# Performance work log

Measured on AMD Instinct MI355X. Metric: run time of the kernel, lower is better.

Reference implementation:

```python
import jax, jax.numpy as jnp
import numpy as np

N_NODES = 100000
N_EDGES = 1600000
D = 8                      # node_channels_in = [D, D]
PROD = D * D               # 64
MSG_DIM = 128
IN_MSG = 2 * PROD + 2 * 2 + 2 * 1   # 134
MSG_OUT = 2 * D            # 16
IN_EIG = 2 * D + 2 * D     # node_channels_sum + 2*D = 32


def setup_inputs() -> dict:
    key = jax.random.key(0)
    ks = jax.random.split(key, 12)
    a = jax.random.normal(ks[0], (N_NODES, D, D), dtype=jnp.float32)
    h_i = 0.5 * (a + jnp.swapaxes(a, -1, -2))  # symmetric so eigh is valid
    edge_index = jax.random.randint(ks[1], (2, N_EDGES), 0, N_NODES)
    node_params = jax.random.normal(ks[2], (N_NODES, 2), dtype=jnp.float32)
    edge_params = jax.random.normal(ks[3], (N_EDGES, 1), dtype=jnp.float32)
    s = 0.05
    return {
        "h_i": h_i,
        "node_params": node_params,
        "edge_params": edge_params,
        "W1": jax.random.normal(ks[4], (IN_MSG, MSG_DIM), dtype=jnp.float32) * s,
        "b1": jnp.zeros((MSG_DIM,), dtype=jnp.float32),
        "W2": jax.random.normal(ks[5], (MSG_DIM, MSG_OUT), dtype=jnp.float32) * s,
        "b2": jnp.zeros((MSG_OUT,), dtype=jnp.float32),
        "W3": jax.random.normal(ks[6], (IN_EIG, MSG_DIM), dtype=jnp.float32) * s,
        "b3": jnp.zeros((MSG_DIM,), dtype=jnp.float32),
        "W4": jax.random.normal(ks[7], (MSG_DIM, D), dtype=jnp.float32) * s,
        "b4": jnp.zeros((D,), dtype=jnp.float32),
        "edge_index": edge_index,
    }


def reference(h_i, node_params, edge_params, W1, b1, W2, b2, W3, b3, W4, b4, edge_index):
    sender = edge_index[0]
    receiver = edge_index[1]
    E = sender.shape[0]
    N = node_params.shape[0]

    # gather + flatten node states per edge: [E, D*D]
    h_s = h_i[sender].reshape(E, -1)
    h_r = h_i[receiver].reshape(E, -1)
    # faithful to torch: edge_params[edge_index] -> [2, E, 1] then view(E, -1) -> [E, 2]
    ep = edge_params[edge_index].reshape(E, -1)

    cat = jnp.concatenate(
        [h_s, h_r, node_params[sender], node_params[receiver], ep], axis=1
    )  # [E, 134]

    # phi_message_Real: Linear -> SiLU -> Linear -> SiLU
    hidden = jax.nn.silu(cat @ W1 + b1)          # [E, 128]
    I_ij = jax.nn.silu(hidden @ W2 + b2)         # [E, 16]

    # scatter_add over receiver
    agg = jax.ops.segment_sum(I_ij, receiver, num_segments=N)  # [N, 16]

    # eigh-based update
    eigvals, eigvecs = jnp.linalg.eigh(h_i)          # [N, D], [N, D, D]
    mags = jnp.linalg.norm(eigvecs, axis=-1)         # [N, D] (row norms, as torch.norm(dim=-1))

    feats = jnp.concatenate([agg, eigvals, mags], axis=1)  # [N, 32]
    lam = jax.nn.softmax(jax.nn.silu(feats @ W3 + b3) @ W4 + b4, axis=-1)  # [N, D]

    # V diag(lam) V^T  per node
    h_updated = jnp.einsum("nij,nj,nkj->nik", eigvecs, lam, eigvecs)
    return h_updated
```

## Files before the change

### kernel.cpp

```cpp
#include <hip/hip_runtime.h>
#include <math.h>

typedef __attribute__((ext_vector_type(8))) short bf16x8;
typedef __attribute__((ext_vector_type(4))) float f32x4;
typedef _Float16 half2v __attribute__((ext_vector_type(2)));

__device__ __forceinline__ float silu(float x) {
    return x / (1.0f + __expf(-x));
}

__device__ __forceinline__ unsigned short f2bf(float x) {
    union { float f; unsigned u; } v; v.f = x;
    unsigned r = v.u + 0x7fffu + ((v.u >> 16) & 1u);
    return (unsigned short)(r >> 16);
}

__device__ __forceinline__ unsigned pack2(float a, float b) {
    return (unsigned)f2bf(a) | ((unsigned)f2bf(b) << 16);
}

__device__ __forceinline__ unsigned pack2h(float a, float b) {
    half2v h; h[0] = (_Float16)a; h[1] = (_Float16)b;
    return __builtin_bit_cast(unsigned, h);
}

__device__ __forceinline__ unsigned cvt_pk(float lo, float hi) {
    unsigned r;
    asm("v_cvt_pk_bf16_f32 %0, %1, %2" : "=v"(r) : "v"(lo), "v"(hi));
    return r;
}

__global__ __launch_bounds__(256)
void k_prep(const float* __restrict__ np,
            const float* __restrict__ ep,
            const int* __restrict__ eidx,
            unsigned* __restrict__ npp,
            unsigned* __restrict__ epk,
            int N, int E)
{
    const int tid = blockIdx.x * 256 + threadIdx.x;
    const int gs = gridDim.x * 256;
    for (int i = tid; i < N; i += gs)
        npp[i] = pack2(np[2 * i], np[2 * i + 1]);
    for (int i = tid; i < E; i += gs)
        epk[i] = pack2h(ep[eidx[2 * i]], ep[eidx[2 * i + 1]]);
}

__global__ __launch_bounds__(256)
void k_pre(const float* __restrict__ h_i,
           const unsigned* __restrict__ npp,
           const float* __restrict__ W1, const float* __restrict__ b1,
           unsigned short* __restrict__ SAB, int N)
{
    const int t = threadIdx.x;
    const int lane = t & 63;
    const int wv = t >> 6;
    const int lr = lane & 15;
    const int lq = lane >> 4;

    bf16x8 aw[4][3];
    #pragma unroll
    for (int mf = 0; mf < 4; ++mf) {
        const int c = wv * 64 + mf * 16 + lr;
        const bool isA = c < 128;
        const int col = c & 127;
        #pragma unroll
        for (int ks = 0; ks < 3; ++ks) {
            bf16x8 w;
            #pragma unroll
            for (int j = 0; j < 8; ++j) {
                const int kl = lq * 8 + j;
                float v = 0.0f;
                if (ks < 2) {
                    const int kk = ks * 32 + kl;
                    v = W1[(size_t)(isA ? kk : 64 + kk) * 128 + col];
                } else if (kl < 2) {
                    v = W1[(size_t)((isA ? 128 : 130) + kl) * 128 + col];
                }
                w[j] = (short)f2bf(v);
            }
            aw[mf][ks] = w;
        }
    }
    float4 b1v[4];
    #pragma unroll
    for (int mf = 0; mf < 4; ++mf) {
        if (wv < 2) b1v[mf] = *(const float4*)&b1[wv * 64 + mf * 16 + lq * 4];
        else        b1v[mf] = make_float4(0.f, 0.f, 0.f, 0.f);
    }

    const int nTiles = (N + 15) / 16;
    for (int tile = blockIdx.x; tile < nTiles; tile += gridDim.x) {
        const int n  = tile * 16 + lr;
        const int nc = (n < N) ? n : (N - 1);

        const float* hr = h_i + (size_t)nc * 64;
        bf16x8 B0, B1, B2;
        {
            float4 a0 = *(const float4*)&hr[lq * 8];
            float4 a1 = *(const float4*)&hr[lq * 8 + 4];
            float4 a2 = *(const float4*)&hr[32 + lq * 8];
            float4 a3 = *(const float4*)&hr[32 + lq * 8 + 4];
            unsigned u[4];
            u[0] = pack2(a0.x, a0.y); u[1] = pack2(a0.z, a0.w);
            u[2] = pack2(a1.x, a1.y); u[3] = pack2(a1.z, a1.w);
            B0 = __builtin_bit_cast(bf16x8, *(uint4*)u);
            u[0] = pack2(a2.x, a2.y); u[1] = pack2(a2.z, a2.w);
            u[2] = pack2(a3.x, a3.y); u[3] = pack2(a3.z, a3.w);
            B1 = __builtin_bit_cast(bf16x8, *(uint4*)u);
            unsigned z[4] = {0u, 0u, 0u, 0u};
            if (lq == 0) z[0] = npp[nc];
            B2 = __builtin_bit_cast(bf16x8, *(uint4*)z);
        }

        f32x4 acc[4];
        #pragma unroll
        for (int mf = 0; mf < 4; ++mf) {
            acc[mf] = (f32x4){0.f, 0.f, 0.f, 0.f};
            acc[mf] = __builtin_amdgcn_mfma_f32_16x16x32_bf16(aw[mf][0], B0, acc[mf], 0, 0, 0);
            acc[mf] = __builtin_amdgcn_mfma_f32_16x16x32_bf16(aw[mf][1], B1, acc[mf], 0, 0, 0);
            acc[mf] = __builtin_amdgcn_mfma_f32_16x16x32_bf16(aw[mf][2], B2, acc[mf], 0, 0, 0);
        }

        if (n < N) {
            unsigned short* row = SAB + (size_t)n * 256;
            #pragma unroll
            for (int mf = 0; mf < 4; ++mf) {
                uint2 u;
                u.x = pack2h(acc[mf][0] + b1v[mf].x, acc[mf][1] + b1v[mf].y);
                u.y = pack2h(acc[mf][2] + b1v[mf].z, acc[mf][3] + b1v[mf].w);
                *(uint2*)&row[wv * 64 + mf * 16 + lq * 4] = u;
            }
        }
    }
}

__global__ __launch_bounds__(256, 3)
void k_edge_v5(const unsigned short* __restrict__ SAB,
               const unsigned* __restrict__ epk,
               const int* __restrict__ eidx,
               const float* __restrict__ W1,
               const float* __restrict__ W2, const float* __restrict__ b2,
               float* __restrict__ agg,
               int N, int E)
{
    const int t = threadIdx.x;
    const int lane = t & 63;
    const int wv = t >> 6;
    const int lr = lane & 15;
    const int lq = lane >> 4;

    half2v wA[4][4], wB[4][4];
    #pragma unroll
    for (int ks = 0; ks < 4; ++ks)
        #pragma unroll
        for (int c = 0; c < 4; ++c) {
            const int d = ks * 32 + lq * 8 + 2 * c;
            half2v a; a[0] = (_Float16)W1[132 * 128 + d]; a[1] = (_Float16)W1[132 * 128 + d + 1];
            half2v b; b[0] = (_Float16)W1[133 * 128 + d]; b[1] = (_Float16)W1[133 * 128 + d + 1];
            wA[ks][c] = a; wB[ks][c] = b;
        }

    bf16x8 bw2[4];
    #pragma unroll
    for (int ks = 0; ks < 4; ++ks) {
        bf16x8 w;
        #pragma unroll
        for (int j = 0; j < 8; ++j) {
            const int k = ks * 32 + lq * 8 + j;
            w[j] = (short)f2bf(W2[(size_t)k * 16 + lr]);
        }
        bw2[ks] = w;
    }
    const float bias2 = b2[lr];

    const uint4* S4 = (const uint4*)SAB;
    const int nG = (E + 15) / 16;
    const int gstride = gridDim.x * 4;
    int g = blockIdx.x * 4 + wv;
    if (g >= nG) return;

    int s0, r0; unsigned ep0; int rc0[4];
    uint4 A0[4], B0[4];
    {
        const int eb = g * 16;
        const int e = eb + lr; const int ec = (e < E) ? e : (E - 1);
        s0 = eidx[ec]; r0 = eidx[E + ec]; ep0 = epk[ec];
        if (eb + 16 <= E) {
            const int4 rv = *(const int4*)&eidx[E + eb + lq * 4];
            rc0[0] = rv.x; rc0[1] = rv.y; rc0[2] = rv.z; rc0[3] = rv.w;
        } else {
            #pragma unroll
            for (int r2 = 0; r2 < 4; ++r2) {
                int e4 = eb + lq * 4 + r2;
                rc0[r2] = eidx[E + ((e4 < E) ? e4 : (E - 1))];
            }
        }
        const uint4* pa = S4 + (size_t)s0 * 32;
        const uint4* pb = S4 + (size_t)r0 * 32 + 16;
        #pragma unroll
        for (int ks = 0; ks < 4; ++ks) { A0[ks] = pa[ks * 4 + lq]; B0[ks] = pb[ks * 4 + lq]; }
    }

    for (; g < nG; g += gstride) {
        const int gn = g + gstride;
        const bool hn = gn < nG;

        int s1 = 0, r1 = 0; unsigned ep1 = 0; int rc1[4] = {0, 0, 0, 0};
        if (hn) {
            const int eb = gn * 16;
            const int e = eb + lr; const int ec = (e < E) ? e : (E - 1);
            s1 = eidx[ec]; r1 = eidx[E + ec]; ep1 = epk[ec];
            if (eb + 16 <= E) {
                const int4 rv = *(const int4*)&eidx[E + eb + lq * 4];
                rc1[0] = rv.x; rc1[1] = rv.y; rc1[2] = rv.z; rc1[3] = rv.w;
            } else {
                #pragma unroll
                for (int r2 = 0; r2 < 4; ++r2) {
                    int e4 = eb + lq * 4 + r2;
                    rc1[r2] = eidx[E + ((e4 < E) ? e4 : (E - 1))];
                }
            }
        }

        const unsigned elo = (ep0 & 0xffffu) | (ep0 << 16);
        const unsigned ehi = (ep0 >> 16) | (ep0 & 0xffff0000u);
        const half2v e0 = __builtin_bit_cast(half2v, elo);
        const half2v e1 = __builtin_bit_cast(half2v, ehi);

        bf16x8 af[4];
        #pragma unroll
        for (int ks = 0; ks < 4; ++ks) {
            unsigned w[4];
            const unsigned* ua = (const unsigned*)&A0[ks];
            const unsigned* ub = (const unsigned*)&B0[ks];
            #pragma unroll
            for (int c = 0; c < 4; ++c) {
                half2v v = __builtin_bit_cast(half2v, ua[c])
                         + __builtin_bit_cast(half2v, ub[c]);
                v = wA[ks][c] * e0 + v;
                v = wB[ks][c] * e1 + v;
                const float x0 = (float)v[0];
                const float x1 = (float)v[1];
                w[c] = cvt_pk(silu(x0), silu(x1));
            }
            af[ks] = __builtin_bit_cast(bf16x8, *(uint4*)w);
        }

        uint4 A1[4], B1[4];
        if (hn) {
            const uint4* pa = S4 + (size_t)s1 * 32;
            const uint4* pb = S4 + (size_t)r1 * 32 + 16;
            #pragma unroll
            for (int ks = 0; ks < 4; ++ks) { A1[ks] = pa[ks * 4 + lq]; B1[ks] = pb[ks * 4 + lq]; }
        }

        f32x4 acc = (f32x4){0.f, 0.f, 0.f, 0.f};
        #pragma unroll
        for (int ks = 0; ks < 4; ++ks)
            acc = __builtin_amdgcn_mfma_f32_16x16x32_bf16(af[ks], bw2[ks], acc, 0, 0, 0);

        const int eb = g * 16;
        if (eb + 16 <= E) {
            #pragma unroll
            for (int r2 = 0; r2 < 4; ++r2)
                atomicAdd(&agg[(size_t)rc0[r2] * 16 + lr], silu(acc[r2] + bias2));
        } else {
            #pragma unroll
            for (int r2 = 0; r2 < 4; ++r2)
                if (eb + lq * 4 + r2 < E)
                    atomicAdd(&agg[(size_t)rc0[r2] * 16 + lr], silu(acc[r2] + bias2));
        }

        if (hn) {
            s0 = s1; r0 = r1; ep0 = ep1;
            #pragma unroll
            for (int r2 = 0; r2 < 4; ++r2) rc0[r2] = rc1[r2];
            #pragma unroll
            for (int ks = 0; ks < 4; ++ks) { A0[ks] = A1[ks]; B0[ks] = B1[ks]; }
        }
    }
}

__host__ __device__ constexpr int tix(int i, int j) {
    return (i <= j) ? (i * 8 - (i * (i + 1)) / 2 + j)
                    : (j * 8 - (j * (j + 1)) / 2 + i);
}

template <int P, int Q>
__device__ __forceinline__ void jrot(float* T, float* V) {
    const float app = T[tix(P, P)];
    const float aqq = T[tix(Q, Q)];
    const float apq = T[tix(P, Q)];

    float theta = (aqq - app) / (2.0f * apq);
    float at = fabsf(theta);
    float tt = 1.0f / (at + sqrtf(at * at + 1.0f));
    tt = (theta < 0.0f) ? -tt : tt;
    float cc = __frsqrt_rn(tt * tt + 1.0f);
    float ss = tt * cc;

    const bool skip = !(fabsf(apq) > 1e-36f);
    const float c  = skip ? 1.0f : cc;
    const float s  = skip ? 0.0f : ss;
    const float tu = skip ? 0.0f : tt;

    #pragma unroll
    for (int k = 0; k < 8; ++k) {
        if (k == P || k == Q) continue;
        const float akp = T[tix(k, P)], akq = T[tix(k, Q)];
        T[tix(k, P)] = c * akp - s * akq;
        T[tix(k, Q)] = s * akp + c * akq;
    }
    T[tix(P, P)] = app - tu * apq;
    T[tix(Q, Q)] = aqq + tu * apq;
    T[tix(P, Q)] = 0.0f;

    #pragma unroll
    for (int k = 0; k < 8; ++k) {
        const float vp = V[k * 8 + P], vq = V[k * 8 + Q];
        V[k * 8 + P] = c * vp - s * vq;
        V[k * 8 + Q] = s * vp + c * vq;
    }
}

__device__ __forceinline__ void jacobi_sweep(float* T, float* V) {
    jrot<0,1>(T,V); jrot<0,2>(T,V); jrot<0,3>(T,V); jrot<0,4>(T,V);
    jrot<0,5>(T,V); jrot<0,6>(T,V); jrot<0,7>(T,V);
    jrot<1,2>(T,V); jrot<1,3>(T,V); jrot<1,4>(T,V); jrot<1,5>(T,V);
    jrot<1,6>(T,V); jrot<1,7>(T,V);
    jrot<2,3>(T,V); jrot<2,4>(T,V); jrot<2,5>(T,V); jrot<2,6>(T,V);
    jrot<2,7>(T,V);
    jrot<3,4>(T,V); jrot<3,5>(T,V); jrot<3,6>(T,V); jrot<3,7>(T,V);
    jrot<4,5>(T,V); jrot<4,6>(T,V); jrot<4,7>(T,V);
    jrot<5,6>(T,V); jrot<5,7>(T,V);
    jrot<6,7>(T,V);
}

#define CSWAP(a, b)                                                          \
    {                                                                        \
        bool sw = eig[a] > eig[b];                                           \
        float lo = sw ? eig[b] : eig[a];                                     \
        float hi = sw ? eig[a] : eig[b];                                     \
        eig[a] = lo; eig[b] = hi;                                            \
        _Pragma("unroll")                                                    \
        for (int k = 0; k < 8; ++k) {                                        \
            float va = V[k * 8 + a], vb = V[k * 8 + b];                      \
            V[k * 8 + a] = sw ? vb : va;                                     \
            V[k * 8 + b] = sw ? va : vb;                                     \
        }                                                                    \
    }

__global__ __launch_bounds__(64)
void k_node(const float* __restrict__ h_i,
            const float* __restrict__ agg,
            const float* __restrict__ W3, const float* __restrict__ b3,
            const float* __restrict__ W4, const float* __restrict__ b4,
            float* __restrict__ out, int N)
{
    const int n = blockIdx.x * 64 + threadIdx.x;
    if (n >= N) return;

    float T[36], V[64];
    {
        float A[64];
        const float4* src = (const float4*)(h_i + (size_t)n * 64);
        #pragma unroll
        for (int i = 0; i < 16; ++i) ((float4*)A)[i] = src[i];
        #pragma unroll
        for (int i = 0; i < 8; ++i)
            #pragma unroll
            for (int j = 0; j < 8; ++j)
                if (i <= j) T[tix(i, j)] = A[i * 8 + j];
    }
    #pragma unroll
    for (int i = 0; i < 64; ++i) V[i] = 0.0f;
    #pragma unroll
    for (int i = 0; i < 8; ++i) V[i * 8 + i] = 1.0f;

    #pragma unroll 1
    for (int sw = 0; sw < 5; ++sw) jacobi_sweep(T, V);

    float eig[8];
    #pragma unroll
    for (int i = 0; i < 8; ++i) eig[i] = T[tix(i, i)];

    CSWAP(0,1) CSWAP(2,3) CSWAP(4,5) CSWAP(6,7)
    CSWAP(0,2) CSWAP(1,3) CSWAP(4,6) CSWAP(5,7)
    CSWAP(1,2) CSWAP(5,6)
    CSWAP(0,4) CSWAP(1,5) CSWAP(2,6) CSWAP(3,7)
    CSWAP(2,4) CSWAP(3,5)
    CSWAP(1,2) CSWAP(3,4) CSWAP(5,6)

    float f[32];
    {
        const float4* ag = (const float4*)(agg + (size_t)n * 16);
        #pragma unroll
        for (int i = 0; i < 4; ++i) {
            float4 v = ag[i];
            f[i * 4 + 0] = v.x; f[i * 4 + 1] = v.y;
            f[i * 4 + 2] = v.z; f[i * 4 + 3] = v.w;
        }
    }
    #pragma unroll
    for (int i = 0; i < 8; ++i) f[16 + i] = eig[i];
    #pragma unroll
    for (int i = 0; i < 8; ++i) f[24 + i] = 1.0f;

    float z[8];
    #pragma unroll
    for (int o = 0; o < 8; ++o) z[o] = b4[o];
    #pragma unroll 1
    for (int j = 0; j < 128; ++j) {
        float h = b3[j];
        #pragma unroll
        for (int k = 0; k < 32; ++k) h += f[k] * W3[k * 128 + j];
        const float sv = silu(h);
        #pragma unroll
        for (int o = 0; o < 8; ++o) z[o] += sv * W4[j * 8 + o];
    }

    float m = z[0];
    #pragma unroll
    for (int o = 1; o < 8; ++o) m = fmaxf(m, z[o]);
    float lam[8], den = 0.0f;
    #pragma unroll
    for (int o = 0; o < 8; ++o) { lam[o] = __expf(z[o] - m); den += lam[o]; }
    const float inv = 1.0f / den;
    #pragma unroll
    for (int o = 0; o < 8; ++o) lam[o] *= inv;

    float* orow = out + (size_t)n * 64;
    #pragma unroll
    for (int i = 0; i < 8; ++i) {
        float si[8];
        #pragma unroll
        for (int j = 0; j < 8; ++j) si[j] = lam[j] * V[i * 8 + j];
        float r[8];
        #pragma unroll
        for (int k = 0; k < 8; ++k) {
            float sum = 0.0f;
            #pragma unroll
            for (int j = 0; j < 8; ++j) sum += si[j] * V[k * 8 + j];
            r[k] = sum;
        }
        ((float4*)orow)[i * 2 + 0] = make_float4(r[0], r[1], r[2], r[3]);
        ((float4*)orow)[i * 2 + 1] = make_float4(r[4], r[5], r[6], r[7]);
    }
}

#define CATS 168
#define HS   136
__global__ __launch_bounds__(256, 2)
void k_edge_v2(const float* __restrict__ h_i,
               const float* __restrict__ node_params,
               const float* __restrict__ edge_params,
               const float* __restrict__ W1, const float* __restrict__ b1,
               const float* __restrict__ W2, const float* __restrict__ b2,
               const int* __restrict__ eidx,
               float* __restrict__ agg,
               int N, int E)
{
    __shared__ unsigned short smem[23680];
    unsigned short* w1t = smem;
    unsigned short* w2t = smem + 128 * CATS;
    unsigned short* cat = smem;
    unsigned short* hid = smem + 64 * CATS;

    const int t = threadIdx.x;
    const int lane = t & 63;
    const int wv = t >> 6;
    const int wn = wv & 1;
    const int wm = wv >> 1;
    const int lr = lane & 15;
    const int lq = lane >> 4;

    for (int idx = t; idx < 128 * 80; idx += 256) {
        const int col = idx & 127, kp = idx >> 7;
        const int k0 = 2 * kp;
        float f0 = (k0     < 134) ? W1[(size_t)k0       * 128 + col] : 0.0f;
        float f1 = (k0 + 1 < 134) ? W1[(size_t)(k0 + 1) * 128 + col] : 0.0f;
        *(unsigned*)&w1t[col * CATS + k0] = pack2(f0, f1);
    }
    for (int idx = t; idx < 16 * 64; idx += 256) {
        const int col = idx & 15, kp = idx >> 4;
        const int k0 = 2 * kp;
        *(unsigned*)&w2t[col * HS + k0] =
            pack2(W2[(size_t)k0 * 16 + col], W2[(size_t)(k0 + 1) * 16 + col]);
    }
    __syncthreads();

    bf16x8 bw1[4][5];
    #pragma unroll
    for (int nf = 0; nf < 4; ++nf)
        #pragma unroll
        for (int ks = 0; ks < 5; ++ks)
            bw1[nf][ks] = *(const bf16x8*)&w1t[(wn * 64 + nf * 16 + lr) * CATS + ks * 32 + lq * 8];
    bf16x8 bw2[4];
    #pragma unroll
    for (int ks = 0; ks < 4; ++ks)
        bw2[ks] = *(const bf16x8*)&w2t[lr * HS + ks * 32 + lq * 8];

    float bias1[4];
    #pragma unroll
    for (int nf = 0; nf < 4; ++nf) bias1[nf] = b1[wn * 64 + nf * 16 + lr];
    const float bias2 = b2[lr];
    __syncthreads();

    const int el = t >> 2;
    const int p  = t & 3;

    const int nTiles = E / 64;
    for (int tile = blockIdx.x; tile < nTiles; tile += gridDim.x) {
        const int ebase = tile * 64;
        {
            const int eg  = ebase + el;
            const int egc = (eg < E) ? eg : (E - 1);
            const int s = eidx[egc];
            const int r = eidx[E + egc];
            const float4* hs = (const float4*)(h_i + (size_t)s * 64);
            const float4* hr = (const float4*)(h_i + (size_t)r * 64);
            unsigned short* crow = cat + el * CATS;
            #pragma unroll
            for (int m = 0; m < 8; ++m) {
                const int q = p + 4 * m;
                float4 v = (q < 16) ? hs[q] : hr[q - 16];
                uint2 u; u.x = pack2(v.x, v.y); u.y = pack2(v.z, v.w);
                *(uint2*)&crow[q * 4] = u;
            }
            if (p == 0) {
                const int i0 = eidx[2 * egc];
                const int i1 = eidx[2 * egc + 1];
                uint4 u;
                u.x = pack2(node_params[2 * s], node_params[2 * s + 1]);
                u.y = pack2(node_params[2 * r], node_params[2 * r + 1]);
                u.z = pack2(edge_params[i0], edge_params[i1]);
                u.w = 0u;
                *(uint4*)&crow[128] = u;
            } else {
                uint4 z; z.x = z.y = z.z = z.w = 0u;
                *(uint4*)&crow[136 + (p - 1) * 8] = z;
            }
        }
        __syncthreads();

        f32x4 acc[2][4];
        #pragma unroll
        for (int mf = 0; mf < 2; ++mf)
            #pragma unroll
            for (int nf = 0; nf < 4; ++nf)
                acc[mf][nf] = (f32x4){0.f, 0.f, 0.f, 0.f};

        const unsigned short* pa = cat + (wm * 32 + lr) * CATS + lq * 8;
        #pragma unroll
        for (int ks = 0; ks < 5; ++ks) {
            const bf16x8 a0 = *(const bf16x8*)(pa + ks * 32);
            const bf16x8 a1 = *(const bf16x8*)(pa + 16 * CATS + ks * 32);
            #pragma unroll
            for (int nf = 0; nf < 4; ++nf) {
                acc[0][nf] = __builtin_amdgcn_mfma_f32_16x16x32_bf16(a0, bw1[nf][ks], acc[0][nf], 0, 0, 0);
                acc[1][nf] = __builtin_amdgcn_mfma_f32_16x16x32_bf16(a1, bw1[nf][ks], acc[1][nf], 0, 0, 0);
            }
        }
        __syncthreads();

        #pragma unroll
        for (int mf = 0; mf < 2; ++mf)
            #pragma unroll
            for (int nf = 0; nf < 4; ++nf) {
                const float bb = bias1[nf];
                #pragma unroll
                for (int r2 = 0; r2 < 4; ++r2) {
                    const float x = acc[mf][nf][r2] + bb;
                    hid[(wm * 32 + mf * 16 + lq * 4 + r2) * HS + wn * 64 + nf * 16 + lr] =
                        f2bf(silu(x));
                }
            }
        __syncthreads();

        f32x4 acc2 = (f32x4){0.f, 0.f, 0.f, 0.f};
        const unsigned short* ph = hid + (wv * 16 + lr) * HS + lq * 8;
        #pragma unroll
        for (int ks = 0; ks < 4; ++ks)
            acc2 = __builtin_amdgcn_mfma_f32_16x16x32_bf16(
                *(const bf16x8*)(ph + ks * 32), bw2[ks], acc2, 0, 0, 0);

        #pragma unroll
        for (int r2 = 0; r2 < 4; ++r2) {
            const int eg2 = ebase + wv * 16 + lq * 4 + r2;
            if (eg2 < E) {
                const int rcv = eidx[E + eg2];
                const float v = silu(acc2[r2] + bias2);
                atomicAdd(&agg[(size_t)rcv * 16 + lr], v);
            }
        }
        __syncthreads();
    }
}

extern "C" void kernel_launch(void* const* d_in, const int* in_sizes, int n_in,
                              void* d_out, int out_size, void* d_ws, size_t ws_size,
                              hipStream_t stream) {
    const float* h_i  = (const float*)d_in[0];
    const float* npar = (const float*)d_in[1];
    const float* epar = (const float*)d_in[2];
    const float* W1   = (const float*)d_in[3];
    const float* b1   = (const float*)d_in[4];
    const float* W2   = (const float*)d_in[5];
    const float* b2   = (const float*)d_in[6];
    const float* W3   = (const float*)d_in[7];
    const float* b3   = (const float*)d_in[8];
    const float* W4   = (const float*)d_in[9];
    const float* b4   = (const float*)d_in[10];
    const int*   eidx = (const int*)d_in[11];

    const int N = in_sizes[0] / 64;
    const int E = in_sizes[11] / 2;

    const size_t aggB = (size_t)N * 16 * sizeof(float);
    size_t off = (aggB + 255) & ~(size_t)255;
    const size_t sabOff = off;                  off += (size_t)N * 256 * 2;
    off = (off + 255) & ~(size_t)255;
    const size_t epkOff = off;                  off += (size_t)E * 4;
    off = (off + 255) & ~(size_t)255;
    const size_t nppOff = off;                  off += (size_t)N * 4;
    const size_t need = off;

    float* agg = (float*)d_ws;
    hipMemsetAsync(agg, 0, aggB, stream);

    if (ws_size >= need) {
        unsigned short* SAB = (unsigned short*)((char*)d_ws + sabOff);
        unsigned* epk = (unsigned*)((char*)d_ws + epkOff);
        unsigned* npp = (unsigned*)((char*)d_ws + nppOff);

        k_prep<<<1024, 256, 0, stream>>>(npar, epar, eidx, npp, epk, N, E);
        k_pre<<<1024, 256, 0, stream>>>(h_i, npp, W1, b1, SAB, N);
        k_edge_v5<<<768, 256, 0, stream>>>(SAB, epk, eidx, W1, W2, b2,
                                           agg, N, E);
    } else {
        int blocks = E / 64;
        if (blocks > 768) blocks = 768;
        k_edge_v2<<<blocks, 256, 0, stream>>>(h_i, npar, epar, W1, b1, W2, b2,
                                              eidx, agg, N, E);
    }
    k_node<<<(N + 63) / 64, 64, 0, stream>>>(h_i, agg, W3, b3, W4, b4,
                                             (float*)d_out, N);
}
```

Measured before the change: 323.7 us.

## Use MFMA for node MLP, merge prep kernels, enlarge edge grid

The per-node scalar MLP (32→128→8) in the node kernel is replaced with fp16 MFMA tiles staged through shared memory, with 256-thread blocks. k_prep and k_pre are merged into one launch whose extra blocks pack the edge params, and node params are packed inline, which drops the npp buffer. The edge kernel grid grows from 768 to 2048 blocks. fp16 weights and activations in the node MLP cost precision, and the larger node blocks may hurt occupancy given the heavy Jacobi register use.

```diff
diff --git a/kernel.cpp b/kernel.cpp
--- a/kernel.cpp
+++ b/kernel.cpp
@@ -4,6 +4,7 @@
 typedef __attribute__((ext_vector_type(8))) short bf16x8;
 typedef __attribute__((ext_vector_type(4))) float f32x4;
 typedef _Float16 half2v __attribute__((ext_vector_type(2)));
+typedef _Float16 f16x8 __attribute__((ext_vector_type(8)));
 
 __device__ __forceinline__ float silu(float x) {
     return x / (1.0f + __expf(-x));
@@ -31,27 +32,23 @@
 }
 
 __global__ __launch_bounds__(256)
-void k_prep(const float* __restrict__ np,
+void k_pre2(const float* __restrict__ h_i,
+            const float* __restrict__ np,
             const float* __restrict__ ep,
             const int* __restrict__ eidx,
-            unsigned* __restrict__ npp,
+            const float* __restrict__ W1, const float* __restrict__ b1,
+            unsigned short* __restrict__ SAB,
             unsigned* __restrict__ epk,
             int N, int E)
 {
-    const int tid = blockIdx.x * 256 + threadIdx.x;
-    const int gs = gridDim.x * 256;
-    for (int i = tid; i < N; i += gs)
-        npp[i] = pack2(np[2 * i], np[2 * i + 1]);
-    for (int i = tid; i < E; i += gs)
-        epk[i] = pack2h(ep[eidx[2 * i]], ep[eidx[2 * i + 1]]);
-}
-
-__global__ __launch_bounds__(256)
-void k_pre(const float* __restrict__ h_i,
-           const unsigned* __restrict__ npp,
-           const float* __restrict__ W1, const float* __restrict__ b1,
-           unsigned short* __restrict__ SAB, int N)
-{
+    if (blockIdx.x >= 1024) {
+        const int tid = (blockIdx.x - 1024) * 256 + threadIdx.x;
+        const int gs = 512 * 256;
+        for (int i = tid; i < E; i += gs)
+            epk[i] = pack2h(ep[eidx[2 * i]], ep[eidx[2 * i + 1]]);
+        return;
+    }
+
     const int t = threadIdx.x;
     const int lane = t & 63;
     const int wv = t >> 6;
@@ -90,7 +87,7 @@
     }
 
     const int nTiles = (N + 15) / 16;
-    for (int tile = blockIdx.x; tile < nTiles; tile += gridDim.x) {
+    for (int tile = blockIdx.x; tile < nTiles; tile += 1024) {
         const int n  = tile * 16 + lr;
         const int nc = (n < N) ? n : (N - 1);
 
@@ -109,7 +106,7 @@
             u[2] = pack2(a3.x, a3.y); u[3] = pack2(a3.z, a3.w);
             B1 = __builtin_bit_cast(bf16x8, *(uint4*)u);
             unsigned z[4] = {0u, 0u, 0u, 0u};
-            if (lq == 0) z[0] = npp[nc];
+            if (lq == 0) z[0] = pack2(np[2 * nc], np[2 * nc + 1]);
             B2 = __builtin_bit_cast(bf16x8, *(uint4*)z);
         }
 
@@ -351,20 +348,30 @@
         }                                                                    \
     }
 
-__global__ __launch_bounds__(64)
-void k_node(const float* __restrict__ h_i,
-            const float* __restrict__ agg,
-            const float* __restrict__ W3, const float* __restrict__ b3,
-            const float* __restrict__ W4, const float* __restrict__ b4,
-            float* __restrict__ out, int N)
+__global__ __launch_bounds__(256)
+void k_node2(const float* __restrict__ h_i,
+             const float* __restrict__ agg,
+             const float* __restrict__ W3, const float* __restrict__ b3,
+             const float* __restrict__ W4, const float* __restrict__ b4,
+             float* __restrict__ out, int N)
 {
-    const int n = blockIdx.x * 64 + threadIdx.x;
-    if (n >= N) return;
+    __shared__ _Float16 fl[4][64][40];
+    __shared__ _Float16 hl[4][16][136];
+    __shared__ float    zl[4][64][8];
+
+    const int t = threadIdx.x;
+    const int lane = t & 63;
+    const int wv = t >> 6;
+    const int lr = lane & 15;
+    const int lq = lane >> 4;
+
+    const int n  = blockIdx.x * 256 + t;
+    const int nc = (n < N) ? n : (N - 1);
 
     float T[36], V[64];
     {
         float A[64];
-        const float4* src = (const float4*)(h_i + (size_t)n * 64);
+        const float4* src = (const float4*)(h_i + (size_t)nc * 64);
         #pragma unroll
         for (int i = 0; i < 16; ++i) ((float4*)A)[i] = src[i];
         #pragma unroll
@@ -392,34 +399,89 @@
     CSWAP(2,4) CSWAP(3,5)
     CSWAP(1,2) CSWAP(3,4) CSWAP(5,6)
 
-    float f[32];
+    f16x8 w3f[8];
+    #pragma unroll
+    for (int nf = 0; nf < 8; ++nf) {
+        f16x8 w;
+        #pragma unroll
+        for (int j = 0; j < 8; ++j)
+            w[j] = (_Float16)W3[(size_t)(lq * 8 + j) * 128 + nf * 16 + lr];
+        w3f[nf] = w;
+    }
+    f16x8 w4f[4];
+    #pragma unroll
+    for (int ks = 0; ks < 4; ++ks) {
+        f16x8 w;
+        #pragma unroll
+        for (int j = 0; j < 8; ++j)
+            w[j] = (lr < 8) ? (_Float16)W4[(size_t)(ks * 32 + lq * 8 + j) * 8 + lr]
+                            : (_Float16)0.0f;
+        w4f[ks] = w;
+    }
+    float b3v[8];
+    #pragma unroll
+    for (int nf = 0; nf < 8; ++nf) b3v[nf] = b3[nf * 16 + lr];
+    const float b4v = (lr < 8) ? b4[lr] : 0.0f;
+
     {
-        const float4* ag = (const float4*)(agg + (size_t)n * 16);
+        float f[32];
+        const float4* ag = (const float4*)(agg + (size_t)nc * 16);
         #pragma unroll
         for (int i = 0; i < 4; ++i) {
             float4 v = ag[i];
             f[i * 4 + 0] = v.x; f[i * 4 + 1] = v.y;
             f[i * 4 + 2] = v.z; f[i * 4 + 3] = v.w;
         }
-    }
-    #pragma unroll
-    for (int i = 0; i < 8; ++i) f[16 + i] = eig[i];
-    #pragma unroll
-    for (int i = 0; i < 8; ++i) f[24 + i] = 1.0f;
+        #pragma unroll
+        for (int i = 0; i < 8; ++i) f[16 + i] = eig[i];
+        #pragma unroll
+        for (int i = 0; i < 8; ++i) f[24 + i] = 1.0f;
+
+        unsigned* dst = (unsigned*)&fl[wv][lane][0];
+        #pragma unroll
+        for (int i = 0; i < 16; ++i) dst[i] = pack2h(f[2 * i], f[2 * i + 1]);
+    }
+    __syncthreads();
+
+    #pragma unroll 1
+    for (int b = 0; b < 4; ++b) {
+        const f16x8 a1 = *(const f16x8*)&fl[wv][b * 16 + lr][lq * 8];
+        f32x4 acc1[8];
+        #pragma unroll
+        for (int nf = 0; nf < 8; ++nf) {
+            acc1[nf] = (f32x4){0.f, 0.f, 0.f, 0.f};
+            acc1[nf] = __builtin_amdgcn_mfma_f32_16x16x32_f16(a1, w3f[nf], acc1[nf], 0, 0, 0);
+        }
+        #pragma unroll
+        for (int nf = 0; nf < 8; ++nf)
+            #pragma unroll
+            for (int r2 = 0; r2 < 4; ++r2) {
+                const float x = acc1[nf][r2] + b3v[nf];
+                hl[wv][lq * 4 + r2][nf * 16 + lr] = (_Float16)silu(x);
+            }
+        __syncthreads();
+
+        f32x4 acc2 = (f32x4){0.f, 0.f, 0.f, 0.f};
+        #pragma unroll
+        for (int ks = 0; ks < 4; ++ks) {
+            const f16x8 a2 = *(const f16x8*)&hl[wv][lr][ks * 32 + lq * 8];
+            acc2 = __builtin_amdgcn_mfma_f32_16x16x32_f16(a2, w4f[ks], acc2, 0, 0, 0);
+        }
+        if (lr < 8) {
+            #pragma unroll
+            for (int r2 = 0; r2 < 4; ++r2)
+                zl[wv][b * 16 + lq * 4 + r2][lr] = acc2[r2] + b4v;
+        }
+        __syncthreads();
+    }
 
     float z[8];
-    #pragma unroll
-    for (int o = 0; o < 8; ++o) z[o] = b4[o];
-    #pragma unroll 1
-    for (int j = 0; j < 128; ++j) {
-        float h = b3[j];
-        #pragma unroll
-        for (int k = 0; k < 32; ++k) h += f[k] * W3[k * 128 + j];
-        const float sv = silu(h);
-        #pragma unroll
-        for (int o = 0; o < 8; ++o) z[o] += sv * W4[j * 8 + o];
-    }
-
+    {
+        float4 z0 = *(const float4*)&zl[wv][lane][0];
+        float4 z1 = *(const float4*)&zl[wv][lane][4];
+        z[0] = z0.x; z[1] = z0.y; z[2] = z0.z; z[3] = z0.w;
+        z[4] = z1.x; z[5] = z1.y; z[6] = z1.z; z[7] = z1.w;
+    }
     float m = z[0];
     #pragma unroll
     for (int o = 1; o < 8; ++o) m = fmaxf(m, z[o]);
@@ -430,22 +492,24 @@
     #pragma unroll
     for (int o = 0; o < 8; ++o) lam[o] *= inv;
 
-    float* orow = out + (size_t)n * 64;
-    #pragma unroll
-    for (int i = 0; i < 8; ++i) {
-        float si[8];
-        #pragma unroll
-        for (int j = 0; j < 8; ++j) si[j] = lam[j] * V[i * 8 + j];
-        float r[8];
-        #pragma unroll
-        for (int k = 0; k < 8; ++k) {
-            float sum = 0.0f;
-            #pragma unroll
-            for (int j = 0; j < 8; ++j) sum += si[j] * V[k * 8 + j];
-            r[k] = sum;
-        }
-        ((float4*)orow)[i * 2 + 0] = make_float4(r[0], r[1], r[2], r[3]);
-        ((float4*)orow)[i * 2 + 1] = make_float4(r[4], r[5], r[6], r[7]);
+    if (n < N) {
+        float* orow = out + (size_t)n * 64;
+        #pragma unroll
+        for (int i = 0; i < 8; ++i) {
+            float si[8];
+            #pragma unroll
+            for (int j = 0; j < 8; ++j) si[j] = lam[j] * V[i * 8 + j];
+            float r[8];
+            #pragma unroll
+            for (int k = 0; k < 8; ++k) {
+                float sum = 0.0f;
+                #pragma unroll
+                for (int j = 0; j < 8; ++j) sum += si[j] * V[k * 8 + j];
+                r[k] = sum;
+            }
+            ((float4*)orow)[i * 2 + 0] = make_float4(r[0], r[1], r[2], r[3]);
+            ((float4*)orow)[i * 2 + 1] = make_float4(r[4], r[5], r[6], r[7]);
+        }
     }
 }
 
@@ -622,8 +686,6 @@
     const size_t sabOff = off;                  off += (size_t)N * 256 * 2;
     off = (off + 255) & ~(size_t)255;
     const size_t epkOff = off;                  off += (size_t)E * 4;
-    off = (off + 255) & ~(size_t)255;
-    const size_t nppOff = off;                  off += (size_t)N * 4;
     const size_t need = off;
 
     float* agg = (float*)d_ws;
@@ -632,18 +694,17 @@
     if (ws_size >= need) {
         unsigned short* SAB = (unsigned short*)((char*)d_ws + sabOff);
         unsigned* epk = (unsigned*)((char*)d_ws + epkOff);
-        unsigned* npp = (unsigned*)((char*)d_ws + nppOff);
-
-        k_prep<<<1024, 256, 0, stream>>>(npar, epar, eidx, npp, epk, N, E);
-        k_pre<<<1024, 256, 0, stream>>>(h_i, npp, W1, b1, SAB, N);
-        k_edge_v5<<<768, 256, 0, stream>>>(SAB, epk, eidx, W1, W2, b2,
-                                           agg, N, E);
+
+        k_pre2<<<1536, 256, 0, stream>>>(h_i, npar, epar, eidx, W1, b1,
+                                         SAB, epk, N, E);
+        k_edge_v5<<<2048, 256, 0, stream>>>(SAB, epk, eidx, W1, W2, b2,
+                                            agg, N, E);
     } else {
         int blocks = E / 64;
         if (blocks > 768) blocks = 768;
         k_edge_v2<<<blocks, 256, 0, stream>>>(h_i, npar, epar, W1, b1, W2, b2,
                                               eidx, agg, N, E);
     }
-    k_node<<<(N + 63) / 64, 64, 0, stream>>>(h_i, agg, W3, b3, W4, b4,
-                                             (float*)d_out, N);
-}
+    k_node2<<<(N + 255) / 256, 256, 0, stream>>>(h_i, agg, W3, b3, W4, b4,
+                                                 (float*)d_out, N);
+}
```

Measured after the change: 285.6 us. 1.13x faster.
